# Kernel tuning notes

Measured on AMD Instinct MI355X. Metric: run time of the kernel, lower is better.

Reference implementation:

```python
import jax, jax.numpy as jnp
import numpy as np

D = 512  # input_channels
K = 64   # centers_num


def setup_inputs() -> dict:
    key = jax.random.key(0)
    k1, k2, k3, k4 = jax.random.split(key, 4)
    inputs = jax.random.normal(k1, (32, D, 56, 56), dtype=jnp.float32)
    # conv 1x1 weight/bias (nn.Conv2d(input_channels, centers_num, (1,1)))
    conv_w = jax.random.normal(k2, (K, D), dtype=jnp.float32) * (1.0 / np.sqrt(D))
    conv_b = jax.random.normal(k3, (K,), dtype=jnp.float32) * 0.01
    # centers ~ U(-0.1, 0.1), shape [D, K]
    centers = jax.random.uniform(k4, (D, K), dtype=jnp.float32, minval=-0.1, maxval=0.1)
    return {"inputs": inputs, "conv_w": conv_w, "conv_b": conv_b, "centers": centers}


def reference(inputs, conv_w, conv_b, centers):
    B, d, H, W = inputs.shape
    N = H * W
    x = inputs.reshape(B, d, N)                      # [B,D,N]
    # 1x1 conv == per-pixel linear: logits [B,K,N]
    logits = jnp.einsum('kd,bdn->bkn', conv_w, x) + conv_b[None, :, None]
    alpha = jax.nn.softmax(logits, axis=1)           # softmax over K (dim=1)
    # vlad[b,d,k] = sum_n alpha[b,k,n] * (x[b,d,n] - centers[d,k])
    vlad = jnp.einsum('bkn,bdn->bdk', alpha, x) - centers[None] * alpha.sum(axis=2)[:, None, :]
    # intra-normalize over D (torch.norm default p=2, no eps)
    vlad = vlad / jnp.linalg.norm(vlad, axis=1, keepdims=True)
    vlad = vlad.reshape(B, d * K)
    vlad = vlad / jnp.linalg.norm(vlad, axis=1, keepdims=True)
    return vlad
```

## Files before the change

kernel.cpp:

```cpp
#include <hip/hip_runtime.h>
#include <math.h>


#define NN 3136
#define DD 512
#define KK 64
#define BB 32

typedef short bf16x8 __attribute__((ext_vector_type(8)));
typedef float f32x4  __attribute__((ext_vector_type(4)));

#define SEL_HI 0x05040100u
#define SEL_LO 0x07060302u

union FragU { uint4 u; bf16x8 f; };

static __device__ inline bf16x8 frag4(unsigned a, unsigned b, unsigned c, unsigned d) {
    FragU x; x.u = make_uint4(a, b, c, d); return x.f;
}

static __device__ inline unsigned pack_split(float f) {
    unsigned u = __float_as_uint(f);
    float hif = __uint_as_float(u & 0xFFFF0000u);
    unsigned lo = __float_as_uint(f - hif) >> 16;
    return (u >> 16) | (lo << 16);
}

static __device__ inline unsigned short bf16_rne(float f) {
    unsigned u = __float_as_uint(f);
    return (unsigned short)((u + 0x7FFFu + ((u >> 16) & 1u)) >> 16);
}

__global__ __launch_bounds__(256) void wprep_kernel(
    const float* __restrict__ w, unsigned* __restrict__ wp)
{
    int i = blockIdx.x * 256 + threadIdx.x;
    wp[i] = pack_split(w[i]);
}

__global__ __launch_bounds__(256) void logits_softmax_mfma(
    const float* __restrict__ x,
    const unsigned* __restrict__ wprep,
    const float* __restrict__ bias,
    unsigned short* __restrict__ alpha)
{
    const int b  = blockIdx.y;
    const int n0 = blockIdx.x * 128;
    const int t  = threadIdx.x;
    const int lane = t & 63;
    const int wv   = t >> 6;
    const int c = lane & 15;
    const int q = lane >> 4;

    __shared__ __align__(16) unsigned xs[128][36];
    __shared__ __align__(16) unsigned ws[64][36];

    f32x4 acc[4][2];
    #pragma unroll
    for (int mt = 0; mt < 4; mt++)
        #pragma unroll
        for (int r = 0; r < 4; r++) {
            float bv = bias[mt * 16 + q * 4 + r];
            acc[mt][0][r] = bv; acc[mt][1][r] = bv;
        }

    const float* xb = x + (size_t)b * DD * NN;
    const int n4 = t & 31;
    const int dr = t >> 5;

    for (int dc = 0; dc < 16; dc++) {
        #pragma unroll
        for (int j = 0; j < 4; j++) {
            int nn = n0 + n4 + 32 * j;
            if (nn > NN - 1) nn = NN - 1;
            unsigned pk[4];
            #pragma unroll
            for (int p = 0; p < 4; p++) {
                float v = xb[(size_t)(dc * 32 + dr * 4 + p) * NN + nn];
                pk[p] = pack_split(v);
            }
            *(uint4*)&xs[n4 + 32 * j][dr * 4] = make_uint4(pk[0], pk[1], pk[2], pk[3]);
        }
        {
            const int row = t >> 2, c4 = t & 3;
            const unsigned* wr = wprep + (size_t)row * DD + dc * 32 + c4 * 8;
            uint4 w0 = *(const uint4*)wr;
            uint4 w1 = *(const uint4*)(wr + 4);
            *(uint4*)&ws[row][c4 * 8]     = w0;
            *(uint4*)&ws[row][c4 * 8 + 4] = w1;
        }
        __syncthreads();

        bf16x8 ah[4], al[4], bh[2], bl[2];
        #pragma unroll
        for (int mt = 0; mt < 4; mt++) {
            uint4 p0 = *(const uint4*)&ws[mt * 16 + c][q * 8];
            uint4 p1 = *(const uint4*)&ws[mt * 16 + c][q * 8 + 4];
            ah[mt] = frag4(__builtin_amdgcn_perm(p0.y, p0.x, SEL_HI),
                           __builtin_amdgcn_perm(p0.w, p0.z, SEL_HI),
                           __builtin_amdgcn_perm(p1.y, p1.x, SEL_HI),
                           __builtin_amdgcn_perm(p1.w, p1.z, SEL_HI));
            al[mt] = frag4(__builtin_amdgcn_perm(p0.y, p0.x, SEL_LO),
                           __builtin_amdgcn_perm(p0.w, p0.z, SEL_LO),
                           __builtin_amdgcn_perm(p1.y, p1.x, SEL_LO),
                           __builtin_amdgcn_perm(p1.w, p1.z, SEL_LO));
        }
        #pragma unroll
        for (int nt = 0; nt < 2; nt++) {
            const int row = wv * 32 + nt * 16 + c;
            uint4 p0 = *(const uint4*)&xs[row][q * 8];
            uint4 p1 = *(const uint4*)&xs[row][q * 8 + 4];
            bh[nt] = frag4(__builtin_amdgcn_perm(p0.y, p0.x, SEL_HI),
                           __builtin_amdgcn_perm(p0.w, p0.z, SEL_HI),
                           __builtin_amdgcn_perm(p1.y, p1.x, SEL_HI),
                           __builtin_amdgcn_perm(p1.w, p1.z, SEL_HI));
            bl[nt] = frag4(__builtin_amdgcn_perm(p0.y, p0.x, SEL_LO),
                           __builtin_amdgcn_perm(p0.w, p0.z, SEL_LO),
                           __builtin_amdgcn_perm(p1.y, p1.x, SEL_LO),
                           __builtin_amdgcn_perm(p1.w, p1.z, SEL_LO));
        }
        #pragma unroll
        for (int mt = 0; mt < 4; mt++)
            #pragma unroll
            for (int nt = 0; nt < 2; nt++) {
                acc[mt][nt] = __builtin_amdgcn_mfma_f32_16x16x32_bf16(ah[mt], bh[nt], acc[mt][nt], 0, 0, 0);
                acc[mt][nt] = __builtin_amdgcn_mfma_f32_16x16x32_bf16(ah[mt], bl[nt], acc[mt][nt], 0, 0, 0);
                acc[mt][nt] = __builtin_amdgcn_mfma_f32_16x16x32_bf16(al[mt], bh[nt], acc[mt][nt], 0, 0, 0);
            }
        __syncthreads();
    }

    unsigned short* ab = alpha + (size_t)b * KK * NN;
    #pragma unroll
    for (int nt = 0; nt < 2; nt++) {
        float mx = -1e30f;
        #pragma unroll
        for (int mt = 0; mt < 4; mt++)
            #pragma unroll
            for (int r = 0; r < 4; r++) mx = fmaxf(mx, acc[mt][nt][r]);
        mx = fmaxf(mx, __shfl_xor(mx, 16));
        mx = fmaxf(mx, __shfl_xor(mx, 32));
        float s = 0.f;
        #pragma unroll
        for (int mt = 0; mt < 4; mt++)
            #pragma unroll
            for (int r = 0; r < 4; r++) {
                float e = __expf(acc[mt][nt][r] - mx);
                acc[mt][nt][r] = e; s += e;
            }
        s += __shfl_xor(s, 16);
        s += __shfl_xor(s, 32);
        const float rinv = 1.0f / s;
        const int pix = n0 + wv * 32 + nt * 16 + c;
        if (pix < NN) {
            #pragma unroll
            for (int mt = 0; mt < 4; mt++)
                #pragma unroll
                for (int r = 0; r < 4; r++)
                    ab[(size_t)(mt * 16 + q * 4 + r) * NN + pix] = bf16_rne(acc[mt][nt][r] * rinv);
        }
    }
}

__global__ __launch_bounds__(64) void asum_kernel(
    const unsigned short* __restrict__ alpha, float* __restrict__ asum)
{
    const int row = blockIdx.x;
    const uint4* p = (const uint4*)(alpha + (size_t)row * NN);
    float s = 0.f;
    for (int j = threadIdx.x; j < 392; j += 64) {
        uint4 v = p[j];
        unsigned a[4] = {v.x, v.y, v.z, v.w};
        #pragma unroll
        for (int i = 0; i < 4; i++)
            s += __uint_as_float(a[i] << 16) + __uint_as_float(a[i] & 0xFFFF0000u);
    }
    #pragma unroll
    for (int off = 32; off; off >>= 1) s += __shfl_down(s, off);
    if (threadIdx.x == 0) asum[row] = s;
}

__global__ __launch_bounds__(256) void vlad_mfma(
    const float* __restrict__ x,
    const unsigned short* __restrict__ alpha,
    float* __restrict__ pvlad,
    int nchunk)
{
    const int dtile = blockIdx.x;
    const int ns    = blockIdx.y;
    const int b     = blockIdx.z;
    const int t     = threadIdx.x;
    const int lane = t & 63;
    const int wv   = t >> 6;
    const int c = lane & 15;
    const int q = lane >> 4;

    __shared__ __align__(16) unsigned short xh[128][40];
    __shared__ __align__(16) unsigned short xl[128][40];
    __shared__ __align__(16) unsigned short as_[64][40];

    f32x4 acc[2][4];
    #pragma unroll
    for (int mt = 0; mt < 2; mt++)
        #pragma unroll
        for (int nt = 0; nt < 4; nt++)
            #pragma unroll
            for (int r = 0; r < 4; r++) acc[mt][nt][r] = 0.f;

    const float* xb = x + ((size_t)b * DD + dtile * 128) * NN;
    const int nchunks = nchunk >> 5;

    for (int cc = 0; cc < nchunks; cc++) {
        const int nb = ns * nchunk + cc * 32;
        {
            const int cg = t & 7, d0 = t >> 3;
            #pragma unroll
            for (int p = 0; p < 4; p++) {
                const int d = d0 + p * 32;
                const int nn = nb + cg * 4;
                float4 v = make_float4(0.f, 0.f, 0.f, 0.f);
                if (nn + 4 <= NN) v = *(const float4*)&xb[(size_t)d * NN + nn];
                unsigned ph[4], pl[4];
                float vv[4] = {v.x, v.y, v.z, v.w};
                #pragma unroll
                for (int i = 0; i < 4; i++) {
                    unsigned pk = pack_split(vv[i]);
                    ph[i] = pk & 0xFFFFu; pl[i] = pk >> 16;
                }
                *(uint2*)&xh[d][cg * 4] = make_uint2(ph[0] | (ph[1] << 16), ph[2] | (ph[3] << 16));
                *(uint2*)&xl[d][cg * 4] = make_uint2(pl[0] | (pl[1] << 16), pl[2] | (pl[3] << 16));
            }
        }
        {
            const int row = t >> 2, c8 = t & 3;
            uint4 av = make_uint4(0u, 0u, 0u, 0u);
            if (nb + c8 * 8 + 8 <= NN)
                av = *(const uint4*)&alpha[((size_t)b * KK + row) * NN + nb + c8 * 8];
            *(uint4*)&as_[row][c8 * 8] = av;
        }
        __syncthreads();

        bf16x8 ah[2], al2[2], bh[4];
        #pragma unroll
        for (int mt = 0; mt < 2; mt++) {
            const int row = wv * 32 + mt * 16 + c;
            ah[mt]  = *(const bf16x8*)&xh[row][q * 8];
            al2[mt] = *(const bf16x8*)&xl[row][q * 8];
        }
        #pragma unroll
        for (int nt = 0; nt < 4; nt++)
            bh[nt] = *(const bf16x8*)&as_[nt * 16 + c][q * 8];

        #pragma unroll
        for (int mt = 0; mt < 2; mt++)
            #pragma unroll
            for (int nt = 0; nt < 4; nt++) {
                acc[mt][nt] = __builtin_amdgcn_mfma_f32_16x16x32_bf16(ah[mt],  bh[nt], acc[mt][nt], 0, 0, 0);
                acc[mt][nt] = __builtin_amdgcn_mfma_f32_16x16x32_bf16(al2[mt], bh[nt], acc[mt][nt], 0, 0, 0);
            }
        __syncthreads();
    }

    float* pv = pvlad + (((size_t)ns * BB + b) * DD + dtile * 128 + wv * 32) * KK;
    #pragma unroll
    for (int mt = 0; mt < 2; mt++)
        #pragma unroll
        for (int r = 0; r < 4; r++) {
            const int dl = mt * 16 + q * 4 + r;
            #pragma unroll
            for (int nt = 0; nt < 4; nt++)
                pv[(size_t)dl * KK + nt * 16 + c] = acc[mt][nt][r];
        }
}

__global__ __launch_bounds__(256) void combine_norm(
    const float* __restrict__ pvlad, const float* __restrict__ centers,
    const float* __restrict__ asum, float* __restrict__ vlad,
    float* __restrict__ psq, int nsplit)
{
    const int dchunk = blockIdx.x;
    const int b = blockIdx.y;
    const int t = threadIdx.x;
    const int k4 = (t & 15) * 4;
    const int dq = t >> 4;
    const float4 av = *(const float4*)&asum[b * KK + k4];
    float sqx = 0.f, sqy = 0.f, sqz = 0.f, sqw = 0.f;
    for (int i = 0; i < 8; i++) {
        const int d = dchunk * 128 + i * 16 + dq;
        float vx = 0.f, vy = 0.f, vz = 0.f, vw = 0.f;
        for (int ns = 0; ns < nsplit; ns++) {
            const float4 p = *(const float4*)&pvlad[(((size_t)ns * BB + b) * DD + d) * KK + k4];
            vx += p.x; vy += p.y; vz += p.z; vw += p.w;
        }
        const float4 cv = *(const float4*)&centers[d * KK + k4];
        vx -= cv.x * av.x; vy -= cv.y * av.y; vz -= cv.z * av.z; vw -= cv.w * av.w;
        *(float4*)&vlad[((size_t)b * DD + d) * KK + k4] = make_float4(vx, vy, vz, vw);
        sqx = fmaf(vx, vx, sqx); sqy = fmaf(vy, vy, sqy);
        sqz = fmaf(vz, vz, sqz); sqw = fmaf(vw, vw, sqw);
    }
    __shared__ float red[16][64];
    red[dq][k4 + 0] = sqx; red[dq][k4 + 1] = sqy;
    red[dq][k4 + 2] = sqz; red[dq][k4 + 3] = sqw;
    __syncthreads();
    if (t < 64) {
        float s = 0.f;
        #pragma unroll
        for (int qq = 0; qq < 16; qq++) s += red[qq][t];
        psq[(b * 4 + dchunk) * 64 + t] = s;
    }
}

__global__ __launch_bounds__(64) void colnorm_final(
    const float* __restrict__ psq, float* __restrict__ cninv)
{
    const int b = blockIdx.x, k = threadIdx.x;
    float s = psq[b * 256 + k] + psq[b * 256 + 64 + k]
            + psq[b * 256 + 128 + k] + psq[b * 256 + 192 + k];
    cninv[b * 64 + k] = 1.0f / (sqrtf(s) * 8.0f);
}

__global__ __launch_bounds__(256) void scale_out(
    const float* __restrict__ vlad, const float* __restrict__ cninv,
    float* __restrict__ out)
{
    const int i4 = (blockIdx.x * 256 + threadIdx.x) * 4;
    float4 v = *(const float4*)&vlad[i4];
    const int b = i4 >> 15;
    const int k = i4 & 63;
    float4 cv = *(const float4*)&cninv[b * KK + k];
    *(float4*)&out[i4] = make_float4(v.x * cv.x, v.y * cv.y, v.z * cv.z, v.w * cv.w);
}

extern "C" void kernel_launch(void* const* d_in, const int* in_sizes, int n_in,
                              void* d_out, int out_size, void* d_ws, size_t ws_size,
                              hipStream_t stream) {
    const float* x       = (const float*)d_in[0];
    const float* conv_w  = (const float*)d_in[1];
    const float* conv_b  = (const float*)d_in[2];
    const float* centers = (const float*)d_in[3];
    float* out = (float*)d_out;

    unsigned* wprep       = (unsigned*)d_ws;
    unsigned short* alpha = (unsigned short*)(wprep + 32768);
    float* asum  = (float*)(alpha + (size_t)BB * KK * NN);
    float* vlad  = asum + 2048;
    float* psq   = vlad + 1048576;
    float* cninv = psq + 8192;
    float* pvlad = cninv + 2048;

    const size_t fixedB = 131072 + 12845056 + (2048 + 1048576 + 8192 + 2048) * 4ull;
    int nsplit = 7;
    if (fixedB + 7ull * 4194304 > ws_size) nsplit = 4;
    if (fixedB + 4ull * 4194304 > ws_size) nsplit = 2;
    if (fixedB + 2ull * 4194304 > ws_size) nsplit = 1;
    const int nchunk = ((NN + nsplit - 1) / nsplit + 31) & ~31;

    wprep_kernel      <<<dim3(128),             dim3(256), 0, stream>>>(conv_w, wprep);
    logits_softmax_mfma<<<dim3(25, BB),         dim3(256), 0, stream>>>(x, wprep, conv_b, alpha);
    asum_kernel       <<<dim3(BB * KK),         dim3(64),  0, stream>>>(alpha, asum);
    vlad_mfma         <<<dim3(4, nsplit, BB),   dim3(256), 0, stream>>>(x, alpha, pvlad, nchunk);
    combine_norm      <<<dim3(4, BB),           dim3(256), 0, stream>>>(pvlad, centers, asum, vlad, psq, nsplit);
    colnorm_final     <<<dim3(BB),              dim3(64),  0, stream>>>(psq, cninv);
    scale_out         <<<dim3(1024),            dim3(256), 0, stream>>>(vlad, cninv, out);
}
```

Before: 375.3 us.

## Fuse alpha column-sum into softmax, presplit weights, widen vlad K-chunk, merge finalize

The conv weights are pre-split into separate hi and lo bf16 arrays, so the logits kernel loads MFMA fragments directly instead of permuting bytes. The per-row alpha sums are accumulated inside the softmax kernel with shuffles and atomics, which removes the separate asum pass over alpha. The vlad kernel now processes 64 pixels per LDS stage with a fixed 4-way pixel split, and the column-norm and scale kernels are merged into one. The trade-offs are atomic contention, a fixed split that no longer adapts to workspace size, fewer vlad blocks, and larger LDS use.

```diff
diff --git a/kernel.cpp b/kernel.cpp
--- a/kernel.cpp
+++ b/kernel.cpp
@@ -32,17 +32,23 @@
 }
 
 __global__ __launch_bounds__(256) void wprep_kernel(
-    const float* __restrict__ w, unsigned* __restrict__ wp)
+    const float* __restrict__ w, unsigned short* __restrict__ wh,
+    unsigned short* __restrict__ wl, float* __restrict__ asum)
 {
     int i = blockIdx.x * 256 + threadIdx.x;
-    wp[i] = pack_split(w[i]);
+    unsigned pk = pack_split(w[i]);
+    wh[i] = (unsigned short)(pk & 0xFFFFu);
+    wl[i] = (unsigned short)(pk >> 16);
+    if (blockIdx.x < 8) asum[blockIdx.x * 256 + threadIdx.x] = 0.f;
 }
 
 __global__ __launch_bounds__(256) void logits_softmax_mfma(
     const float* __restrict__ x,
-    const unsigned* __restrict__ wprep,
+    const unsigned short* __restrict__ wh,
+    const unsigned short* __restrict__ wl,
     const float* __restrict__ bias,
-    unsigned short* __restrict__ alpha)
+    unsigned short* __restrict__ alpha,
+    float* __restrict__ asum)
 {
     const int b  = blockIdx.y;
     const int n0 = blockIdx.x * 128;
@@ -53,7 +59,8 @@
     const int q = lane >> 4;
 
     __shared__ __align__(16) unsigned xs[128][36];
-    __shared__ __align__(16) unsigned ws[64][36];
+    __shared__ __align__(16) unsigned short wsh[64][40];
+    __shared__ __align__(16) unsigned short wsl[64][40];
 
     f32x4 acc[4][2];
     #pragma unroll
@@ -82,28 +89,18 @@
             *(uint4*)&xs[n4 + 32 * j][dr * 4] = make_uint4(pk[0], pk[1], pk[2], pk[3]);
         }
         {
-            const int row = t >> 2, c4 = t & 3;
-            const unsigned* wr = wprep + (size_t)row * DD + dc * 32 + c4 * 8;
-            uint4 w0 = *(const uint4*)wr;
-            uint4 w1 = *(const uint4*)(wr + 4);
-            *(uint4*)&ws[row][c4 * 8]     = w0;
-            *(uint4*)&ws[row][c4 * 8 + 4] = w1;
+            const int row = t >> 2, c8 = t & 3;
+            const size_t off = (size_t)row * DD + dc * 32 + c8 * 8;
+            *(uint4*)&wsh[row][c8 * 8] = *(const uint4*)&wh[off];
+            *(uint4*)&wsl[row][c8 * 8] = *(const uint4*)&wl[off];
         }
         __syncthreads();
 
         bf16x8 ah[4], al[4], bh[2], bl[2];
         #pragma unroll
         for (int mt = 0; mt < 4; mt++) {
-            uint4 p0 = *(const uint4*)&ws[mt * 16 + c][q * 8];
-            uint4 p1 = *(const uint4*)&ws[mt * 16 + c][q * 8 + 4];
-            ah[mt] = frag4(__builtin_amdgcn_perm(p0.y, p0.x, SEL_HI),
-                           __builtin_amdgcn_perm(p0.w, p0.z, SEL_HI),
-                           __builtin_amdgcn_perm(p1.y, p1.x, SEL_HI),
-                           __builtin_amdgcn_perm(p1.w, p1.z, SEL_HI));
-            al[mt] = frag4(__builtin_amdgcn_perm(p0.y, p0.x, SEL_LO),
-                           __builtin_amdgcn_perm(p0.w, p0.z, SEL_LO),
-                           __builtin_amdgcn_perm(p1.y, p1.x, SEL_LO),
-                           __builtin_amdgcn_perm(p1.w, p1.z, SEL_LO));
+            ah[mt] = *(const bf16x8*)&wsh[mt * 16 + c][q * 8];
+            al[mt] = *(const bf16x8*)&wsl[mt * 16 + c][q * 8];
         }
         #pragma unroll
         for (int nt = 0; nt < 2; nt++) {
@@ -131,6 +128,12 @@
     }
 
     unsigned short* ab = alpha + (size_t)b * KK * NN;
+    float sa[4][4];
+    #pragma unroll
+    for (int mt = 0; mt < 4; mt++)
+        #pragma unroll
+        for (int r = 0; r < 4; r++) sa[mt][r] = 0.f;
+
     #pragma unroll
     for (int nt = 0; nt < 2; nt++) {
         float mx = -1e30f;
@@ -152,39 +155,38 @@
         s += __shfl_xor(s, 32);
         const float rinv = 1.0f / s;
         const int pix = n0 + wv * 32 + nt * 16 + c;
-        if (pix < NN) {
-            #pragma unroll
-            for (int mt = 0; mt < 4; mt++)
-                #pragma unroll
-                for (int r = 0; r < 4; r++)
-                    ab[(size_t)(mt * 16 + q * 4 + r) * NN + pix] = bf16_rne(acc[mt][nt][r] * rinv);
-        }
-    }
-}
-
-__global__ __launch_bounds__(64) void asum_kernel(
-    const unsigned short* __restrict__ alpha, float* __restrict__ asum)
-{
-    const int row = blockIdx.x;
-    const uint4* p = (const uint4*)(alpha + (size_t)row * NN);
-    float s = 0.f;
-    for (int j = threadIdx.x; j < 392; j += 64) {
-        uint4 v = p[j];
-        unsigned a[4] = {v.x, v.y, v.z, v.w};
-        #pragma unroll
-        for (int i = 0; i < 4; i++)
-            s += __uint_as_float(a[i] << 16) + __uint_as_float(a[i] & 0xFFFF0000u);
-    }
-    #pragma unroll
-    for (int off = 32; off; off >>= 1) s += __shfl_down(s, off);
-    if (threadIdx.x == 0) asum[row] = s;
+        const bool ok = pix < NN;
+        #pragma unroll
+        for (int mt = 0; mt < 4; mt++)
+            #pragma unroll
+            for (int r = 0; r < 4; r++) {
+                unsigned short ub = bf16_rne(acc[mt][nt][r] * rinv);
+                if (ok) {
+                    ab[(size_t)(mt * 16 + q * 4 + r) * NN + pix] = ub;
+                    sa[mt][r] += __uint_as_float((unsigned)ub << 16);
+                }
+            }
+    }
+    #pragma unroll
+    for (int off = 1; off <= 8; off <<= 1)
+        #pragma unroll
+        for (int mt = 0; mt < 4; mt++)
+            #pragma unroll
+            for (int r = 0; r < 4; r++)
+                sa[mt][r] += __shfl_xor(sa[mt][r], off);
+    if (c == 0) {
+        #pragma unroll
+        for (int mt = 0; mt < 4; mt++)
+            #pragma unroll
+            for (int r = 0; r < 4; r++)
+                atomicAdd(&asum[b * KK + mt * 16 + q * 4 + r], sa[mt][r]);
+    }
 }
 
 __global__ __launch_bounds__(256) void vlad_mfma(
     const float* __restrict__ x,
     const unsigned short* __restrict__ alpha,
-    float* __restrict__ pvlad,
-    int nchunk)
+    float* __restrict__ pvlad)
 {
     const int dtile = blockIdx.x;
     const int ns    = blockIdx.y;
@@ -195,9 +197,9 @@
     const int c = lane & 15;
     const int q = lane >> 4;
 
-    __shared__ __align__(16) unsigned short xh[128][40];
-    __shared__ __align__(16) unsigned short xl[128][40];
-    __shared__ __align__(16) unsigned short as_[64][40];
+    __shared__ __align__(16) unsigned short xh[128][72];
+    __shared__ __align__(16) unsigned short xl[128][72];
+    __shared__ __align__(16) unsigned short as_[64][72];
 
     f32x4 acc[2][4];
     #pragma unroll
@@ -208,56 +210,60 @@
             for (int r = 0; r < 4; r++) acc[mt][nt][r] = 0.f;
 
     const float* xb = x + ((size_t)b * DD + dtile * 128) * NN;
-    const int nchunks = nchunk >> 5;
-
-    for (int cc = 0; cc < nchunks; cc++) {
-        const int nb = ns * nchunk + cc * 32;
-        {
-            const int cg = t & 7, d0 = t >> 3;
-            #pragma unroll
-            for (int p = 0; p < 4; p++) {
-                const int d = d0 + p * 32;
-                const int nn = nb + cg * 4;
-                float4 v = make_float4(0.f, 0.f, 0.f, 0.f);
-                if (nn + 4 <= NN) v = *(const float4*)&xb[(size_t)d * NN + nn];
-                unsigned ph[4], pl[4];
-                float vv[4] = {v.x, v.y, v.z, v.w};
+    const int nq = t & 15, dr2 = t >> 4;
+    const int arow = t >> 2, ac = t & 3;
+
+    const int nchunk = 784;
+    for (int cc = 0; cc < 13; cc++) {
+        const int nb = ns * nchunk + cc * 64;
+        const int nvalid = min(64, nchunk - cc * 64);
+        #pragma unroll
+        for (int p = 0; p < 8; p++) {
+            const int d = dr2 + p * 16;
+            uint2 h = make_uint2(0u, 0u), l = make_uint2(0u, 0u);
+            if (nq * 4 < nvalid) {
+                float4 v = *(const float4*)&xb[(size_t)d * NN + nb + nq * 4];
+                unsigned pk0 = pack_split(v.x), pk1 = pack_split(v.y);
+                unsigned pk2 = pack_split(v.z), pk3 = pack_split(v.w);
+                h.x = __builtin_amdgcn_perm(pk1, pk0, SEL_HI);
+                h.y = __builtin_amdgcn_perm(pk3, pk2, SEL_HI);
+                l.x = __builtin_amdgcn_perm(pk1, pk0, SEL_LO);
+                l.y = __builtin_amdgcn_perm(pk3, pk2, SEL_LO);
+            }
+            *(uint2*)&xh[d][nq * 4] = h;
+            *(uint2*)&xl[d][nq * 4] = l;
+        }
+        #pragma unroll
+        for (int j = 0; j < 2; j++) {
+            const int col = ac * 16 + j * 8;
+            uint4 v = make_uint4(0u, 0u, 0u, 0u);
+            if (col < nvalid)
+                v = *(const uint4*)&alpha[((size_t)b * KK + arow) * NN + nb + col];
+            *(uint4*)&as_[arow][col] = v;
+        }
+        __syncthreads();
+
+        #pragma unroll
+        for (int ks = 0; ks < 2; ks++) {
+            const int colb = ks * 32 + q * 8;
+            bf16x8 ah[2], al2[2], bh[4];
+            #pragma unroll
+            for (int mt = 0; mt < 2; mt++) {
+                const int row = wv * 32 + mt * 16 + c;
+                ah[mt]  = *(const bf16x8*)&xh[row][colb];
+                al2[mt] = *(const bf16x8*)&xl[row][colb];
+            }
+            #pragma unroll
+            for (int nt = 0; nt < 4; nt++)
+                bh[nt] = *(const bf16x8*)&as_[nt * 16 + c][colb];
+            #pragma unroll
+            for (int mt = 0; mt < 2; mt++)
                 #pragma unroll
-                for (int i = 0; i < 4; i++) {
-                    unsigned pk = pack_split(vv[i]);
-                    ph[i] = pk & 0xFFFFu; pl[i] = pk >> 16;
+                for (int nt = 0; nt < 4; nt++) {
+                    acc[mt][nt] = __builtin_amdgcn_mfma_f32_16x16x32_bf16(ah[mt],  bh[nt], acc[mt][nt], 0, 0, 0);
+                    acc[mt][nt] = __builtin_amdgcn_mfma_f32_16x16x32_bf16(al2[mt], bh[nt], acc[mt][nt], 0, 0, 0);
                 }
-                *(uint2*)&xh[d][cg * 4] = make_uint2(ph[0] | (ph[1] << 16), ph[2] | (ph[3] << 16));
-                *(uint2*)&xl[d][cg * 4] = make_uint2(pl[0] | (pl[1] << 16), pl[2] | (pl[3] << 16));
-            }
-        }
-        {
-            const int row = t >> 2, c8 = t & 3;
-            uint4 av = make_uint4(0u, 0u, 0u, 0u);
-            if (nb + c8 * 8 + 8 <= NN)
-                av = *(const uint4*)&alpha[((size_t)b * KK + row) * NN + nb + c8 * 8];
-            *(uint4*)&as_[row][c8 * 8] = av;
-        }
-        __syncthreads();
-
-        bf16x8 ah[2], al2[2], bh[4];
-        #pragma unroll
-        for (int mt = 0; mt < 2; mt++) {
-            const int row = wv * 32 + mt * 16 + c;
-            ah[mt]  = *(const bf16x8*)&xh[row][q * 8];
-            al2[mt] = *(const bf16x8*)&xl[row][q * 8];
-        }
-        #pragma unroll
-        for (int nt = 0; nt < 4; nt++)
-            bh[nt] = *(const bf16x8*)&as_[nt * 16 + c][q * 8];
-
-        #pragma unroll
-        for (int mt = 0; mt < 2; mt++)
-            #pragma unroll
-            for (int nt = 0; nt < 4; nt++) {
-                acc[mt][nt] = __builtin_amdgcn_mfma_f32_16x16x32_bf16(ah[mt],  bh[nt], acc[mt][nt], 0, 0, 0);
-                acc[mt][nt] = __builtin_amdgcn_mfma_f32_16x16x32_bf16(al2[mt], bh[nt], acc[mt][nt], 0, 0, 0);
-            }
+        }
         __syncthreads();
     }
 
@@ -276,7 +282,7 @@
 __global__ __launch_bounds__(256) void combine_norm(
     const float* __restrict__ pvlad, const float* __restrict__ centers,
     const float* __restrict__ asum, float* __restrict__ vlad,
-    float* __restrict__ psq, int nsplit)
+    float* __restrict__ psq)
 {
     const int dchunk = blockIdx.x;
     const int b = blockIdx.y;
@@ -288,7 +294,8 @@
     for (int i = 0; i < 8; i++) {
         const int d = dchunk * 128 + i * 16 + dq;
         float vx = 0.f, vy = 0.f, vz = 0.f, vw = 0.f;
-        for (int ns = 0; ns < nsplit; ns++) {
+        #pragma unroll
+        for (int ns = 0; ns < 4; ns++) {
             const float4 p = *(const float4*)&pvlad[(((size_t)ns * BB + b) * DD + d) * KK + k4];
             vx += p.x; vy += p.y; vz += p.z; vw += p.w;
         }
@@ -310,25 +317,29 @@
     }
 }
 
-__global__ __launch_bounds__(64) void colnorm_final(
-    const float* __restrict__ psq, float* __restrict__ cninv)
-{
-    const int b = blockIdx.x, k = threadIdx.x;
-    float s = psq[b * 256 + k] + psq[b * 256 + 64 + k]
-            + psq[b * 256 + 128 + k] + psq[b * 256 + 192 + k];
-    cninv[b * 64 + k] = 1.0f / (sqrtf(s) * 8.0f);
-}
-
-__global__ __launch_bounds__(256) void scale_out(
-    const float* __restrict__ vlad, const float* __restrict__ cninv,
+__global__ __launch_bounds__(256) void finalize_kernel(
+    const float* __restrict__ psq, const float* __restrict__ vlad,
     float* __restrict__ out)
 {
-    const int i4 = (blockIdx.x * 256 + threadIdx.x) * 4;
-    float4 v = *(const float4*)&vlad[i4];
-    const int b = i4 >> 15;
-    const int k = i4 & 63;
-    float4 cv = *(const float4*)&cninv[b * KK + k];
-    *(float4*)&out[i4] = make_float4(v.x * cv.x, v.y * cv.y, v.z * cv.z, v.w * cv.w);
+    const int dchunk = blockIdx.x;
+    const int b = blockIdx.y;
+    const int t = threadIdx.x;
+    __shared__ float cn[64];
+    if (t < 64) {
+        float s = psq[b * 256 + t] + psq[b * 256 + 64 + t]
+                + psq[b * 256 + 128 + t] + psq[b * 256 + 192 + t];
+        cn[t] = 1.0f / (sqrtf(s) * 8.0f);
+    }
+    __syncthreads();
+    const int k4 = (t & 15) * 4;
+    const int dq = t >> 4;
+    const float4 cv = *(const float4*)&cn[k4];
+    #pragma unroll
+    for (int i = 0; i < 8; i++) {
+        const size_t idx = ((size_t)b * DD + dchunk * 128 + i * 16 + dq) * KK + k4;
+        float4 v = *(const float4*)&vlad[idx];
+        *(float4*)&out[idx] = make_float4(v.x * cv.x, v.y * cv.y, v.z * cv.z, v.w * cv.w);
+    }
 }
 
 extern "C" void kernel_launch(void* const* d_in, const int* in_sizes, int n_in,
@@ -340,26 +351,17 @@
     const float* centers = (const float*)d_in[3];
     float* out = (float*)d_out;
 
-    unsigned* wprep       = (unsigned*)d_ws;
-    unsigned short* alpha = (unsigned short*)(wprep + 32768);
+    unsigned short* wh    = (unsigned short*)d_ws;
+    unsigned short* wl    = wh + 32768;
+    unsigned short* alpha = wl + 32768;
     float* asum  = (float*)(alpha + (size_t)BB * KK * NN);
     float* vlad  = asum + 2048;
     float* psq   = vlad + 1048576;
-    float* cninv = psq + 8192;
-    float* pvlad = cninv + 2048;
-
-    const size_t fixedB = 131072 + 12845056 + (2048 + 1048576 + 8192 + 2048) * 4ull;
-    int nsplit = 7;
-    if (fixedB + 7ull * 4194304 > ws_size) nsplit = 4;
-    if (fixedB + 4ull * 4194304 > ws_size) nsplit = 2;
-    if (fixedB + 2ull * 4194304 > ws_size) nsplit = 1;
-    const int nchunk = ((NN + nsplit - 1) / nsplit + 31) & ~31;
-
-    wprep_kernel      <<<dim3(128),             dim3(256), 0, stream>>>(conv_w, wprep);
-    logits_softmax_mfma<<<dim3(25, BB),         dim3(256), 0, stream>>>(x, wprep, conv_b, alpha);
-    asum_kernel       <<<dim3(BB * KK),         dim3(64),  0, stream>>>(alpha, asum);
-    vlad_mfma         <<<dim3(4, nsplit, BB),   dim3(256), 0, stream>>>(x, alpha, pvlad, nchunk);
-    combine_norm      <<<dim3(4, BB),           dim3(256), 0, stream>>>(pvlad, centers, asum, vlad, psq, nsplit);
-    colnorm_final     <<<dim3(BB),              dim3(64),  0, stream>>>(psq, cninv);
-    scale_out         <<<dim3(1024),            dim3(256), 0, stream>>>(vlad, cninv, out);
-}
+    float* pvlad = psq + 8192;
+
+    wprep_kernel       <<<dim3(128),        dim3(256), 0, stream>>>(conv_w, wh, wl, asum);
+    logits_softmax_mfma<<<dim3(25, BB),     dim3(256), 0, stream>>>(x, wh, wl, conv_b, alpha, asum);
+    vlad_mfma          <<<dim3(4, 4, BB),   dim3(256), 0, stream>>>(x, alpha, pvlad);
+    combine_norm       <<<dim3(4, BB),      dim3(256), 0, stream>>>(pvlad, centers, asum, vlad, psq);
+    finalize_kernel    <<<dim3(4, BB),      dim3(256), 0, stream>>>(psq, vlad, out);
+}
```

Result: no change. 378.1 us (+0.7%).
